# Kernel tuning notes

Measured on AMD Instinct MI355X. Metric: run time of the kernel, lower is better.

The kernel has to match this reference:

```python
import jax, jax.numpy as jnp
import numpy as np

NF = 128  # latent_dim / number of filters


def setup_inputs() -> dict:
    key = jax.random.key(0)
    k1, k2, k3, k4 = jax.random.split(key, 4)
    B, H, W, C = 4, 64, 64, 128
    x = jax.random.normal(k1, (B, H, W, C), dtype=jnp.float32)
    y = jax.random.normal(k2, (B, H, W, C), dtype=jnp.float32)
    # 1x1 conv kernels (C_in, C_out) + biases, glorot-ish scale
    scale = 1.0 / np.sqrt(C)
    W1 = jax.random.normal(k3, (C, NF), dtype=jnp.float32) * scale
    W2 = jax.random.normal(k4, (C, NF), dtype=jnp.float32) * scale
    b1 = jnp.zeros((NF,), dtype=jnp.float32)
    b2 = jnp.zeros((NF,), dtype=jnp.float32)
    return {"x": x, "y": y, "W1": W1, "b1": b1, "W2": W2, "b2": b2}


def reference(x, y, W1, b1, W2, b2):
    B, H, Wd, C = x.shape
    hw = H * Wd
    # 1x1 convs == per-pixel matmul
    xq = jnp.einsum('bhwc,cf->bhwf', x, W1) + b1   # conv1(x)
    yk = jnp.einsum('bhwc,cf->bhwf', y, W2) + b2   # conv2(y)
    xq_r = xq.reshape(B, hw, NF)
    yk_r = yk.reshape(B, hw, NF)
    # A_ij = sigmoid(y_i . x_j), full (hw x hw) sigmoid attention
    A = jax.nn.sigmoid(jnp.einsum('bic,bjc->bij', yk_r, xq_r))
    out = jnp.einsum('bij,bjc->bic', A, yk_r).reshape(B, H, Wd, NF)
    # residual add of the *projected* x (matches original: x was overwritten by conv1)
    out = out + xq
    return out
```

## Files before the change

### kernel.cpp

```cpp
#include <hip/hip_runtime.h>
#include <hip/hip_bf16.h>
#include <stdint.h>

typedef float f32x16 __attribute__((ext_vector_type(16)));
typedef float f32x4  __attribute__((ext_vector_type(4)));
typedef short s16x8  __attribute__((ext_vector_type(8)));
typedef unsigned int u32x4 __attribute__((ext_vector_type(4)));

#define HWSZ   4096
#define NBATCH 4
#define LOG2E  1.44269504088896340736f

__device__ __forceinline__ unsigned short f2bf(float f) {
    unsigned u = __builtin_bit_cast(unsigned, f);
    u += 0x7FFFu + ((u >> 16) & 1u);
    return (unsigned short)(u >> 16);
}
__device__ __forceinline__ unsigned cvt_pk_bf16(float lo, float hi) {
    __hip_bfloat162 h = __float22bfloat162_rn(make_float2(lo, hi));
    return *reinterpret_cast<unsigned*>(&h);
}

__global__ __launch_bounds__(256, 1) void proj_kernel(
    const float* __restrict__ x, const float* __restrict__ y,
    const float* __restrict__ W1, const float* __restrict__ b1,
    const float* __restrict__ W2, const float* __restrict__ b2,
    float* __restrict__ xq_f32,
    unsigned short* __restrict__ xq_bf,
    unsigned short* __restrict__ yk_bf,
    unsigned short* __restrict__ ykT_bf)
{
    __shared__ unsigned short Xlds[64][136];
    __shared__ unsigned short Ylds[64][136];
    __shared__ unsigned short Tlds[128][72];

    const int t    = threadIdx.x;
    const int lane = t & 63;
    const int w    = t >> 6;
    const int l31  = lane & 31;
    const int g    = lane >> 5;
    const int r0   = blockIdx.x * 64;
    const int b    = r0 >> 12;
    const int j0   = r0 & (HWSZ - 1);

    #pragma unroll
    for (int i = 0; i < 8; ++i) {
        int li = t + 256 * i;
        int row = li >> 5, c = (li & 31) * 4;
        float4 vx = *(const float4*)(x + (size_t)(r0 + row) * 128 + c);
        float4 vy = *(const float4*)(y + (size_t)(r0 + row) * 128 + c);
        *(uint2*)&Xlds[row][c] = make_uint2(cvt_pk_bf16(vx.x, vx.y), cvt_pk_bf16(vx.z, vx.w));
        *(uint2*)&Ylds[row][c] = make_uint2(cvt_pk_bf16(vy.x, vy.y), cvt_pk_bf16(vy.z, vy.w));
    }
    __syncthreads();

    const int m  = w >> 1;
    const int fh = w & 1;
    const float* Wm = m ? W2 : W1;
    const float* bm = m ? b2 : b1;
    const unsigned short* A0 = m ? &Ylds[0][0] : &Xlds[0][0];

    f32x16 acc[2][2];
    #pragma unroll
    for (int i = 0; i < 16; ++i) {
        acc[0][0][i] = 0.f; acc[0][1][i] = 0.f;
        acc[1][0][i] = 0.f; acc[1][1][i] = 0.f;
    }

    #pragma unroll
    for (int ks = 0; ks < 8; ++ks) {
        s16x8 bfr[2];
        #pragma unroll
        for (int ft = 0; ft < 2; ++ft) {
            const float* wp = Wm + (size_t)(ks * 16 + g * 8) * 128 + fh * 64 + ft * 32 + l31;
            #pragma unroll
            for (int i = 0; i < 8; ++i)
                bfr[ft][i] = (short)f2bf(wp[(size_t)i * 128]);
        }
        #pragma unroll
        for (int rt = 0; rt < 2; ++rt) {
            s16x8 af = *(const s16x8*)(A0 + (size_t)(rt * 32 + l31) * 136 + ks * 16 + g * 8);
            acc[rt][0] = __builtin_amdgcn_mfma_f32_32x32x16_bf16(af, bfr[0], acc[rt][0], 0, 0, 0);
            acc[rt][1] = __builtin_amdgcn_mfma_f32_32x32x16_bf16(af, bfr[1], acc[rt][1], 0, 0, 0);
        }
    }

    const float bias_v[2] = { bm[fh * 64 + l31], bm[fh * 64 + 32 + l31] };

    if (m == 0) {
        #pragma unroll
        for (int rt = 0; rt < 2; ++rt)
        #pragma unroll
        for (int ft = 0; ft < 2; ++ft) {
            int f = fh * 64 + ft * 32 + l31;
            #pragma unroll
            for (int r = 0; r < 16; ++r) {
                int row = rt * 32 + (r & 3) + 8 * (r >> 2) + 4 * g;
                float v = acc[rt][ft][r] + bias_v[ft];
                size_t o = (size_t)(r0 + row) * 128 + f;
                xq_f32[o] = v;
                xq_bf[o]  = f2bf(v * LOG2E);
            }
        }
    } else {
        #pragma unroll
        for (int rt = 0; rt < 2; ++rt)
        #pragma unroll
        for (int ft = 0; ft < 2; ++ft) {
            int f = fh * 64 + ft * 32 + l31;
            #pragma unroll
            for (int rg = 0; rg < 4; ++rg) {
                float p0 = acc[rt][ft][4 * rg + 0] + bias_v[ft];
                float p1 = acc[rt][ft][4 * rg + 1] + bias_v[ft];
                float p2 = acc[rt][ft][4 * rg + 2] + bias_v[ft];
                float p3 = acc[rt][ft][4 * rg + 3] + bias_v[ft];
                int jb = rt * 32 + 8 * rg + 4 * g;
                *(uint2*)&Tlds[f][jb] = make_uint2(cvt_pk_bf16(p0, p1), cvt_pk_bf16(p2, p3));
                size_t o = (size_t)(r0 + jb) * 128 + f;
                yk_bf[o]       = f2bf(p0);
                yk_bf[o + 128] = f2bf(p1);
                yk_bf[o + 256] = f2bf(p2);
                yk_bf[o + 384] = f2bf(p3);
            }
        }
    }
    __syncthreads();

    {
        int f  = t >> 1;
        int jh = (t & 1) * 32;
        unsigned short* dst = ykT_bf + ((size_t)(b * 128 + f)) * HWSZ + j0 + jh;
        #pragma unroll
        for (int c = 0; c < 4; ++c)
            *(s16x8*)(dst + c * 8) = *(const s16x8*)&Tlds[f][jh + c * 8];
    }
}

#define KT_STR   136
#define VT_STR   72
#define KT_BYTES (64 * KT_STR * 2)
#define VT_BYTES (128 * VT_STR * 2)
#define BUF_BYTES (KT_BYTES + VT_BYTES)

__global__ __launch_bounds__(256, 2) void attn128_kernel(
    const unsigned short* __restrict__ Kbf,
    const unsigned short* __restrict__ Qbf,
    const unsigned short* __restrict__ Vtbf,
    float* __restrict__ outp)
{
    __shared__ __align__(16) char smem[2 * BUF_BYTES];

    const int t    = threadIdx.x;
    const int lane = t & 63;
    const int qt   = t >> 6;
    const int l31  = lane & 31;
    const int g    = lane >> 5;

    const int split  = blockIdx.x >> 7;
    const int r      = blockIdx.x & 127;
    const int b      = r >> 5;
    const int qb     = (r & 31) * 128;
    const int jBegin = split * (HWSZ / 4);
    const int nt     = (HWSZ / 4) / 64;

    s16x8 qfrag[8];
    {
        const unsigned short* qp =
            Qbf + (((size_t)(b * HWSZ + qb + 32 * qt + l31)) << 7) + g * 8;
        #pragma unroll
        for (int fs = 0; fs < 8; ++fs)
            qfrag[fs] = *(const s16x8*)(qp + fs * 16);
    }

    f32x16 acc[4];
    #pragma unroll
    for (int ft = 0; ft < 4; ++ft)
        #pragma unroll
        for (int i = 0; i < 16; ++i) acc[ft][i] = 0.f;

    const unsigned short* Kbase = Kbf  + (((size_t)b * HWSZ) << 7);
    const unsigned short* Vbase = Vtbf + (((size_t)b) << 7) * HWSZ;

    const unsigned short* kSrc = Kbase + (size_t)(jBegin + (t >> 4)) * 128 + (t & 15) * 8;
    const unsigned short* vSrc = Vbase + (size_t)(t >> 3) * HWSZ + jBegin + (t & 7) * 8;
    const int kDst = (t >> 4) * KT_STR + (t & 15) * 8;
    const int vDst = (t >> 3) * VT_STR + (t & 7) * 8;

    {
        unsigned short* Kl = (unsigned short*)smem;
        unsigned short* Vl = (unsigned short*)(smem + KT_BYTES);
        #pragma unroll
        for (int i = 0; i < 4; ++i)
            *(s16x8*)(Kl + kDst + i * 16 * KT_STR) = *(const s16x8*)(kSrc + (size_t)i * 2048);
        #pragma unroll
        for (int i = 0; i < 4; ++i)
            *(s16x8*)(Vl + vDst + i * 32 * VT_STR) = *(const s16x8*)(vSrc + (size_t)i * 32 * HWSZ);
    }
    __syncthreads();

    int c = 0;
    for (int it = 0; it < nt; ++it) {
        const bool pre = (it + 1 < nt);
        s16x8 kr[4], vr[4];
        if (pre) {
            kSrc += 64 * 128;
            vSrc += 64;
            #pragma unroll
            for (int i = 0; i < 4; ++i)
                kr[i] = *(const s16x8*)(kSrc + (size_t)i * 2048);
            #pragma unroll
            for (int i = 0; i < 4; ++i)
                vr[i] = *(const s16x8*)(vSrc + (size_t)i * 32 * HWSZ);
        }

        const unsigned short* Kl = (const unsigned short*)(smem + c * BUF_BYTES);
        const unsigned short* Vl = (const unsigned short*)(smem + c * BUF_BYTES + KT_BYTES);

        #pragma unroll
        for (int jt = 0; jt < 2; ++jt) {
            f32x16 sa, sb;
            #pragma unroll
            for (int i = 0; i < 16; ++i) { sa[i] = 0.f; sb[i] = 0.f; }
            const unsigned short* Krow = Kl + (size_t)(32 * jt + l31) * KT_STR + g * 8;
            __builtin_amdgcn_s_setprio(1);
            #pragma unroll
            for (int fs = 0; fs < 4; ++fs) {
                sa = __builtin_amdgcn_mfma_f32_32x32x16_bf16(
                         *(const s16x8*)(Krow + fs * 16), qfrag[fs], sa, 0, 0, 0);
                sb = __builtin_amdgcn_mfma_f32_32x32x16_bf16(
                         *(const s16x8*)(Krow + (fs + 4) * 16), qfrag[fs + 4], sb, 0, 0, 0);
            }
            __builtin_amdgcn_s_setprio(0);

            unsigned W0[4], W1[4];
            #pragma unroll
            for (int rg = 0; rg < 4; ++rg) {
                float s0 = sa[4 * rg + 0] + sb[4 * rg + 0];
                float s1 = sa[4 * rg + 1] + sb[4 * rg + 1];
                float s2v = sa[4 * rg + 2] + sb[4 * rg + 2];
                float s3 = sa[4 * rg + 3] + sb[4 * rg + 3];
                float p0 = __builtin_amdgcn_rcpf(1.f + __builtin_amdgcn_exp2f(-s0));
                float p1 = __builtin_amdgcn_rcpf(1.f + __builtin_amdgcn_exp2f(-s1));
                float p2 = __builtin_amdgcn_rcpf(1.f + __builtin_amdgcn_exp2f(-s2v));
                float p3 = __builtin_amdgcn_rcpf(1.f + __builtin_amdgcn_exp2f(-s3));
                W0[rg] = cvt_pk_bf16(p0, p1);
                W1[rg] = cvt_pk_bf16(p2, p3);
            }

            #pragma unroll
            for (int s2 = 0; s2 < 2; ++s2) {
                unsigned a0 = W0[2 * s2], b0 = W0[2 * s2 + 1];
                unsigned a1 = W1[2 * s2], b1 = W1[2 * s2 + 1];
                asm("v_permlane32_swap_b32 %0, %1" : "+v"(a0), "+v"(b0));
                asm("v_permlane32_swap_b32 %0, %1" : "+v"(a1), "+v"(b1));
                u32x4 pw;
                pw[0] = a0; pw[1] = a1; pw[2] = b0; pw[3] = b1;
                s16x8 pf = __builtin_bit_cast(s16x8, pw);
                const int ks = 2 * jt + s2;
                __builtin_amdgcn_s_setprio(1);
                #pragma unroll
                for (int ft = 0; ft < 4; ++ft) {
                    s16x8 vf = *(const s16x8*)(Vl + (size_t)(32 * ft + l31) * VT_STR + ks * 16 + g * 8);
                    acc[ft] = __builtin_amdgcn_mfma_f32_32x32x16_bf16(pf, vf, acc[ft], 0, 0, 0);
                }
                __builtin_amdgcn_s_setprio(0);
            }
        }

        if (pre) {
            unsigned short* Kd = (unsigned short*)(smem + (c ^ 1) * BUF_BYTES);
            unsigned short* Vd = (unsigned short*)(smem + (c ^ 1) * BUF_BYTES + KT_BYTES);
            #pragma unroll
            for (int i = 0; i < 4; ++i)
                *(s16x8*)(Kd + kDst + i * 16 * KT_STR) = kr[i];
            #pragma unroll
            for (int i = 0; i < 4; ++i)
                *(s16x8*)(Vd + vDst + i * 32 * VT_STR) = vr[i];
        }
        __syncthreads();
        c ^= 1;
    }

    float* op = outp + (size_t)split * ((size_t)NBATCH * HWSZ * 128);
    #pragma unroll
    for (int ft = 0; ft < 4; ++ft)
    #pragma unroll
    for (int r2 = 0; r2 < 16; ++r2) {
        int row = (r2 & 3) + 8 * (r2 >> 2) + 4 * g;
        int q = qb + 32 * qt + row;
        size_t o = (((size_t)(b * HWSZ + q)) << 7) + 32 * ft + l31;
        op[o] = acc[ft][r2];
    }
}

template<bool SPLIT>
__global__ __launch_bounds__(256, 2) void attn_kernel(
    const unsigned short* __restrict__ Kbf,
    const unsigned short* __restrict__ Qbf,
    const unsigned short* __restrict__ Vtbf,
    const float* __restrict__ resid,
    float* __restrict__ outp)
{
    __shared__ __align__(16) char smem[2 * BUF_BYTES];

    const int t    = threadIdx.x;
    const int lane = t & 63;
    const int w    = t >> 6;
    const int qt   = w & 1;
    const int jt   = w >> 1;
    const int l31  = lane & 31;
    const int g    = lane >> 5;

    int bid = blockIdx.x;
    int half = 0;
    if (SPLIT) { half = bid >> 8; bid &= 255; }
    const int b      = bid >> 6;
    const int qb     = (bid & 63) * 64;
    const int jBegin = half * (HWSZ / 2);
    const int nt     = (SPLIT ? HWSZ / 2 : HWSZ) / 64;

    s16x8 qfrag[8];
    {
        const unsigned short* qp =
            Qbf + (((size_t)(b * HWSZ + qb + 32 * qt + l31)) << 7) + g * 8;
        #pragma unroll
        for (int fs = 0; fs < 8; ++fs)
            qfrag[fs] = *(const s16x8*)(qp + fs * 16);
    }

    f32x16 acc[4];
    #pragma unroll
    for (int ft = 0; ft < 4; ++ft)
        #pragma unroll
        for (int i = 0; i < 16; ++i) acc[ft][i] = 0.f;

    const unsigned short* Kbase = Kbf  + (((size_t)b * HWSZ) << 7);
    const unsigned short* Vbase = Vtbf + (((size_t)b) << 7) * HWSZ;

    const unsigned short* kSrc = Kbase + (size_t)(jBegin + (t >> 4)) * 128 + (t & 15) * 8;
    const unsigned short* vSrc = Vbase + (size_t)(t >> 3) * HWSZ + jBegin + (t & 7) * 8;
    const int kDst = (t >> 4) * KT_STR + (t & 15) * 8;
    const int vDst = (t >> 3) * VT_STR + (t & 7) * 8;

    {
        unsigned short* Kl = (unsigned short*)smem;
        unsigned short* Vl = (unsigned short*)(smem + KT_BYTES);
        #pragma unroll
        for (int i = 0; i < 4; ++i)
            *(s16x8*)(Kl + kDst + i * 16 * KT_STR) = *(const s16x8*)(kSrc + (size_t)i * 2048);
        #pragma unroll
        for (int i = 0; i < 4; ++i)
            *(s16x8*)(Vl + vDst + i * 32 * VT_STR) = *(const s16x8*)(vSrc + (size_t)i * 32 * HWSZ);
    }
    __syncthreads();

    int c = 0;
    for (int it = 0; it < nt; ++it) {
        const bool pre = (it + 1 < nt);
        s16x8 kr[4], vr[4];
        if (pre) {
            kSrc += 64 * 128;
            vSrc += 64;
            #pragma unroll
            for (int i = 0; i < 4; ++i)
                kr[i] = *(const s16x8*)(kSrc + (size_t)i * 2048);
            #pragma unroll
            for (int i = 0; i < 4; ++i)
                vr[i] = *(const s16x8*)(vSrc + (size_t)i * 32 * HWSZ);
        }

        const unsigned short* Kl = (const unsigned short*)(smem + c * BUF_BYTES);
        const unsigned short* Vl = (const unsigned short*)(smem + c * BUF_BYTES + KT_BYTES);

        f32x16 sa, sb;
        #pragma unroll
        for (int i = 0; i < 16; ++i) { sa[i] = 0.f; sb[i] = 0.f; }
        const unsigned short* Krow = Kl + (size_t)(32 * jt + l31) * KT_STR + g * 8;
        __builtin_amdgcn_s_setprio(1);
        #pragma unroll
        for (int fs = 0; fs < 4; ++fs) {
            sa = __builtin_amdgcn_mfma_f32_32x32x16_bf16(
                     *(const s16x8*)(Krow + fs * 16), qfrag[fs], sa, 0, 0, 0);
            sb = __builtin_amdgcn_mfma_f32_32x32x16_bf16(
                     *(const s16x8*)(Krow + (fs + 4) * 16), qfrag[fs + 4], sb, 0, 0, 0);
        }
        __builtin_amdgcn_s_setprio(0);

        unsigned W0[4], W1[4];
        #pragma unroll
        for (int rg = 0; rg < 4; ++rg) {
            float s0 = sa[4 * rg + 0] + sb[4 * rg + 0];
            float s1 = sa[4 * rg + 1] + sb[4 * rg + 1];
            float s2v = sa[4 * rg + 2] + sb[4 * rg + 2];
            float s3 = sa[4 * rg + 3] + sb[4 * rg + 3];
            float p0 = __builtin_amdgcn_rcpf(1.f + __builtin_amdgcn_exp2f(-s0));
            float p1 = __builtin_amdgcn_rcpf(1.f + __builtin_amdgcn_exp2f(-s1));
            float p2 = __builtin_amdgcn_rcpf(1.f + __builtin_amdgcn_exp2f(-s2v));
            float p3 = __builtin_amdgcn_rcpf(1.f + __builtin_amdgcn_exp2f(-s3));
            W0[rg] = cvt_pk_bf16(p0, p1);
            W1[rg] = cvt_pk_bf16(p2, p3);
        }

        #pragma unroll
        for (int s2 = 0; s2 < 2; ++s2) {
            unsigned a0 = W0[2 * s2], b0 = W0[2 * s2 + 1];
            unsigned a1 = W1[2 * s2], b1 = W1[2 * s2 + 1];
            asm("v_permlane32_swap_b32 %0, %1" : "+v"(a0), "+v"(b0));
            asm("v_permlane32_swap_b32 %0, %1" : "+v"(a1), "+v"(b1));
            u32x4 pw;
            pw[0] = a0; pw[1] = a1; pw[2] = b0; pw[3] = b1;
            s16x8 pf = __builtin_bit_cast(s16x8, pw);
            const int ks = 2 * jt + s2;
            __builtin_amdgcn_s_setprio(1);
            #pragma unroll
            for (int ft = 0; ft < 4; ++ft) {
                s16x8 vf = *(const s16x8*)(Vl + (size_t)(32 * ft + l31) * VT_STR + ks * 16 + g * 8);
                acc[ft] = __builtin_amdgcn_mfma_f32_32x32x16_bf16(pf, vf, acc[ft], 0, 0, 0);
            }
            __builtin_amdgcn_s_setprio(0);
        }

        if (pre) {
            unsigned short* Kd = (unsigned short*)(smem + (c ^ 1) * BUF_BYTES);
            unsigned short* Vd = (unsigned short*)(smem + (c ^ 1) * BUF_BYTES + KT_BYTES);
            #pragma unroll
            for (int i = 0; i < 4; ++i)
                *(s16x8*)(Kd + kDst + i * 16 * KT_STR) = kr[i];
            #pragma unroll
            for (int i = 0; i < 4; ++i)
                *(s16x8*)(Vd + vDst + i * 32 * VT_STR) = vr[i];
        }
        __syncthreads();
        c ^= 1;
    }

    float* red = (float*)smem;
    if (jt == 1) {
        #pragma unroll
        for (int ft = 0; ft < 4; ++ft)
        #pragma unroll
        for (int r = 0; r < 16; ++r) {
            int row = (r & 3) + 8 * (r >> 2) + 4 * g;
            red[qt * 4096 + row * 128 + 32 * ft + l31] = acc[ft][r];
        }
    }
    __syncthreads();
    if (jt == 0) {
        float* op = outp + (SPLIT ? (size_t)half * ((size_t)NBATCH * HWSZ * 128) : 0);
        #pragma unroll
        for (int ft = 0; ft < 4; ++ft)
        #pragma unroll
        for (int r = 0; r < 16; ++r) {
            int row = (r & 3) + 8 * (r >> 2) + 4 * g;
            float v = acc[ft][r] + red[qt * 4096 + row * 128 + 32 * ft + l31];
            int q = qb + 32 * qt + row;
            size_t o = (((size_t)(b * HWSZ + q)) << 7) + 32 * ft + l31;
            if (SPLIT) op[o] = v;
            else       op[o] = v + resid[o];
        }
    }
}

__global__ __launch_bounds__(256, 1) void reduce2_kernel(
    const float* __restrict__ p0, const float* __restrict__ p1, float* outp)
{
    int i = blockIdx.x * 256 + threadIdx.x;
    f32x4 a = ((const f32x4*)p0)[i];
    f32x4 b = ((const f32x4*)p1)[i];
    f32x4 c = ((f32x4*)outp)[i];
    ((f32x4*)outp)[i] = a + b + c;
}

template<int S>
__global__ __launch_bounds__(256, 1) void reduceN_kernel(
    const float* __restrict__ parts, float* __restrict__ outp)
{
    const size_t N4 = (size_t)NBATCH * HWSZ * 128 / 4;
    size_t i = (size_t)blockIdx.x * 256 + threadIdx.x;
    f32x4 s = ((f32x4*)outp)[i];
    #pragma unroll
    for (int k = 0; k < S; ++k)
        s += ((const f32x4*)parts)[i + (size_t)k * N4];
    ((f32x4*)outp)[i] = s;
}

extern "C" void kernel_launch(void* const* d_in, const int* in_sizes, int n_in,
                              void* d_out, int out_size, void* d_ws, size_t ws_size,
                              hipStream_t stream) {
    const float* x  = (const float*)d_in[0];
    const float* y  = (const float*)d_in[1];
    const float* W1 = (const float*)d_in[2];
    const float* b1 = (const float*)d_in[3];
    const float* W2 = (const float*)d_in[4];
    const float* b2 = (const float*)d_in[5];
    float* out = (float*)d_out;

    const size_t NELEM = (size_t)NBATCH * HWSZ * 128;
    unsigned short* xq_bf  = (unsigned short*)d_ws;
    unsigned short* yk_bf  = xq_bf + NELEM;
    unsigned short* ykT_bf = yk_bf + NELEM;
    float* part = (float*)(ykT_bf + NELEM);

    proj_kernel<<<(int)(NBATCH * HWSZ / 64), 256, 0, stream>>>(
        x, y, W1, b1, W2, b2, out, xq_bf, yk_bf, ykT_bf);

    if (ws_size >= NELEM * (6 + 16)) {
        attn128_kernel<<<512, 256, 0, stream>>>(xq_bf, yk_bf, ykT_bf, part);
        reduceN_kernel<4><<<(int)(NELEM / 1024), 256, 0, stream>>>(part, out);
    } else if (ws_size >= NELEM * (6 + 8)) {
        attn_kernel<true><<<512, 256, 0, stream>>>(xq_bf, yk_bf, ykT_bf, out, part);
        reduce2_kernel<<<(int)(NELEM / 1024), 256, 0, stream>>>(part, part + NELEM, out);
    } else {
        attn_kernel<false><<<256, 256, 0, stream>>>(xq_bf, yk_bf, ykT_bf, out, out);
    }
}
```

Measured before the change: 69.53 us.

## Split attention key range six ways with single-buffered K to fit three blocks per CU

Adds an attention kernel that splits the key dimension into six uneven chunks (11 or 10 tiles of 64) and launches 768 blocks instead of 512. K shared memory is single-buffered while V stays double-buffered, shrinking LDS so three blocks can reside per CU, and an extra barrier guards the K overwrite. The aim is better CU fill and latency hiding on the 256-CU device. In exchange it writes six fp32 partial outputs and the reduction reads six instead of four, costing extra memory traffic and an added sync per tile. It is only taken when the workspace is large enough.

Measured after the change: 96.87 us. +39.3%, slower.

```diff
diff --git a/kernel.cpp b/kernel.cpp
--- a/kernel.cpp
+++ b/kernel.cpp
@@ -142,13 +142,14 @@
 #define VT_BYTES (128 * VT_STR * 2)
 #define BUF_BYTES (KT_BYTES + VT_BYTES)
 
-__global__ __launch_bounds__(256, 2) void attn128_kernel(
+__global__ __launch_bounds__(256, 3) void attn128s6_kernel(
     const unsigned short* __restrict__ Kbf,
     const unsigned short* __restrict__ Qbf,
     const unsigned short* __restrict__ Vtbf,
     float* __restrict__ outp)
 {
-    __shared__ __align__(16) char smem[2 * BUF_BYTES];
+    __shared__ __align__(16) unsigned short Klds[64 * KT_STR];
+    __shared__ __align__(16) unsigned short Vlds[2][128 * VT_STR];
 
     const int t    = threadIdx.x;
     const int lane = t & 63;
@@ -156,12 +157,13 @@
     const int l31  = lane & 31;
     const int g    = lane >> 5;
 
-    const int split  = blockIdx.x >> 7;
-    const int r      = blockIdx.x & 127;
-    const int b      = r >> 5;
-    const int qb     = (r & 31) * 128;
-    const int jBegin = split * (HWSZ / 4);
-    const int nt     = (HWSZ / 4) / 64;
+    const int split = blockIdx.x >> 7;
+    const int r     = blockIdx.x & 127;
+    const int b     = r >> 5;
+    const int qb    = (r & 31) * 128;
+    const int st    = 11 * split - (split > 4 ? split - 4 : 0);
+    const int nt    = (split >= 4) ? 10 : 11;
+    const int jBegin = st * 64;
 
     s16x8 qfrag[8];
     {
@@ -187,14 +189,12 @@
     const int vDst = (t >> 3) * VT_STR + (t & 7) * 8;
 
     {
-        unsigned short* Kl = (unsigned short*)smem;
-        unsigned short* Vl = (unsigned short*)(smem + KT_BYTES);
         #pragma unroll
         for (int i = 0; i < 4; ++i)
-            *(s16x8*)(Kl + kDst + i * 16 * KT_STR) = *(const s16x8*)(kSrc + (size_t)i * 2048);
+            *(s16x8*)(Klds + kDst + i * 16 * KT_STR) = *(const s16x8*)(kSrc + (size_t)i * 2048);
         #pragma unroll
         for (int i = 0; i < 4; ++i)
-            *(s16x8*)(Vl + vDst + i * 32 * VT_STR) = *(const s16x8*)(vSrc + (size_t)i * 32 * HWSZ);
+            *(s16x8*)(&Vlds[0][0] + vDst + i * 32 * VT_STR) = *(const s16x8*)(vSrc + (size_t)i * 32 * HWSZ);
     }
     __syncthreads();
 
@@ -213,15 +213,14 @@
                 vr[i] = *(const s16x8*)(vSrc + (size_t)i * 32 * HWSZ);
         }
 
-        const unsigned short* Kl = (const unsigned short*)(smem + c * BUF_BYTES);
-        const unsigned short* Vl = (const unsigned short*)(smem + c * BUF_BYTES + KT_BYTES);
+        const unsigned short* Vl = &Vlds[c][0];
 
         #pragma unroll
         for (int jt = 0; jt < 2; ++jt) {
             f32x16 sa, sb;
             #pragma unroll
             for (int i = 0; i < 16; ++i) { sa[i] = 0.f; sb[i] = 0.f; }
-            const unsigned short* Krow = Kl + (size_t)(32 * jt + l31) * KT_STR + g * 8;
+            const unsigned short* Krow = Klds + (size_t)(32 * jt + l31) * KT_STR + g * 8;
             __builtin_amdgcn_s_setprio(1);
             #pragma unroll
             for (int fs = 0; fs < 4; ++fs) {
@@ -267,6 +266,156 @@
             }
         }
 
+        __syncthreads();
+        if (pre) {
+            #pragma unroll
+            for (int i = 0; i < 4; ++i)
+                *(s16x8*)(Klds + kDst + i * 16 * KT_STR) = kr[i];
+            #pragma unroll
+            for (int i = 0; i < 4; ++i)
+                *(s16x8*)(&Vlds[c ^ 1][0] + vDst + i * 32 * VT_STR) = vr[i];
+            __syncthreads();
+        }
+        c ^= 1;
+    }
+
+    float* op = outp + (size_t)split * ((size_t)NBATCH * HWSZ * 128);
+    #pragma unroll
+    for (int ft = 0; ft < 4; ++ft)
+    #pragma unroll
+    for (int r2 = 0; r2 < 16; ++r2) {
+        int row = (r2 & 3) + 8 * (r2 >> 2) + 4 * g;
+        int q = qb + 32 * qt + row;
+        size_t o = (((size_t)(b * HWSZ + q)) << 7) + 32 * ft + l31;
+        op[o] = acc[ft][r2];
+    }
+}
+
+__global__ __launch_bounds__(256, 2) void attn128_kernel(
+    const unsigned short* __restrict__ Kbf,
+    const unsigned short* __restrict__ Qbf,
+    const unsigned short* __restrict__ Vtbf,
+    float* __restrict__ outp)
+{
+    __shared__ __align__(16) char smem[2 * BUF_BYTES];
+
+    const int t    = threadIdx.x;
+    const int lane = t & 63;
+    const int qt   = t >> 6;
+    const int l31  = lane & 31;
+    const int g    = lane >> 5;
+
+    const int split  = blockIdx.x >> 7;
+    const int r      = blockIdx.x & 127;
+    const int b      = r >> 5;
+    const int qb     = (r & 31) * 128;
+    const int jBegin = split * (HWSZ / 4);
+    const int nt     = (HWSZ / 4) / 64;
+
+    s16x8 qfrag[8];
+    {
+        const unsigned short* qp =
+            Qbf + (((size_t)(b * HWSZ + qb + 32 * qt + l31)) << 7) + g * 8;
+        #pragma unroll
+        for (int fs = 0; fs < 8; ++fs)
+            qfrag[fs] = *(const s16x8*)(qp + fs * 16);
+    }
+
+    f32x16 acc[4];
+    #pragma unroll
+    for (int ft = 0; ft < 4; ++ft)
+        #pragma unroll
+        for (int i = 0; i < 16; ++i) acc[ft][i] = 0.f;
+
+    const unsigned short* Kbase = Kbf  + (((size_t)b * HWSZ) << 7);
+    const unsigned short* Vbase = Vtbf + (((size_t)b) << 7) * HWSZ;
+
+    const unsigned short* kSrc = Kbase + (size_t)(jBegin + (t >> 4)) * 128 + (t & 15) * 8;
+    const unsigned short* vSrc = Vbase + (size_t)(t >> 3) * HWSZ + jBegin + (t & 7) * 8;
+    const int kDst = (t >> 4) * KT_STR + (t & 15) * 8;
+    const int vDst = (t >> 3) * VT_STR + (t & 7) * 8;
+
+    {
+        unsigned short* Kl = (unsigned short*)smem;
+        unsigned short* Vl = (unsigned short*)(smem + KT_BYTES);
+        #pragma unroll
+        for (int i = 0; i < 4; ++i)
+            *(s16x8*)(Kl + kDst + i * 16 * KT_STR) = *(const s16x8*)(kSrc + (size_t)i * 2048);
+        #pragma unroll
+        for (int i = 0; i < 4; ++i)
+            *(s16x8*)(Vl + vDst + i * 32 * VT_STR) = *(const s16x8*)(vSrc + (size_t)i * 32 * HWSZ);
+    }
+    __syncthreads();
+
+    int c = 0;
+    for (int it = 0; it < nt; ++it) {
+        const bool pre = (it + 1 < nt);
+        s16x8 kr[4], vr[4];
+        if (pre) {
+            kSrc += 64 * 128;
+            vSrc += 64;
+            #pragma unroll
+            for (int i = 0; i < 4; ++i)
+                kr[i] = *(const s16x8*)(kSrc + (size_t)i * 2048);
+            #pragma unroll
+            for (int i = 0; i < 4; ++i)
+                vr[i] = *(const s16x8*)(vSrc + (size_t)i * 32 * HWSZ);
+        }
+
+        const unsigned short* Kl = (const unsigned short*)(smem + c * BUF_BYTES);
+        const unsigned short* Vl = (const unsigned short*)(smem + c * BUF_BYTES + KT_BYTES);
+
+        #pragma unroll
+        for (int jt = 0; jt < 2; ++jt) {
+            f32x16 sa, sb;
+            #pragma unroll
+            for (int i = 0; i < 16; ++i) { sa[i] = 0.f; sb[i] = 0.f; }
+            const unsigned short* Krow = Kl + (size_t)(32 * jt + l31) * KT_STR + g * 8;
+            __builtin_amdgcn_s_setprio(1);
+            #pragma unroll
+            for (int fs = 0; fs < 4; ++fs) {
+                sa = __builtin_amdgcn_mfma_f32_32x32x16_bf16(
+                         *(const s16x8*)(Krow + fs * 16), qfrag[fs], sa, 0, 0, 0);
+                sb = __builtin_amdgcn_mfma_f32_32x32x16_bf16(
+                         *(const s16x8*)(Krow + (fs + 4) * 16), qfrag[fs + 4], sb, 0, 0, 0);
+            }
+            __builtin_amdgcn_s_setprio(0);
+
+            unsigned W0[4], W1[4];
+            #pragma unroll
+            for (int rg = 0; rg < 4; ++rg) {
+                float s0 = sa[4 * rg + 0] + sb[4 * rg + 0];
+                float s1 = sa[4 * rg + 1] + sb[4 * rg + 1];
+                float s2v = sa[4 * rg + 2] + sb[4 * rg + 2];
+                float s3 = sa[4 * rg + 3] + sb[4 * rg + 3];
+                float p0 = __builtin_amdgcn_rcpf(1.f + __builtin_amdgcn_exp2f(-s0));
+                float p1 = __builtin_amdgcn_rcpf(1.f + __builtin_amdgcn_exp2f(-s1));
+                float p2 = __builtin_amdgcn_rcpf(1.f + __builtin_amdgcn_exp2f(-s2v));
+                float p3 = __builtin_amdgcn_rcpf(1.f + __builtin_amdgcn_exp2f(-s3));
+                W0[rg] = cvt_pk_bf16(p0, p1);
+                W1[rg] = cvt_pk_bf16(p2, p3);
+            }
+
+            #pragma unroll
+            for (int s2 = 0; s2 < 2; ++s2) {
+                unsigned a0 = W0[2 * s2], b0 = W0[2 * s2 + 1];
+                unsigned a1 = W1[2 * s2], b1 = W1[2 * s2 + 1];
+                asm("v_permlane32_swap_b32 %0, %1" : "+v"(a0), "+v"(b0));
+                asm("v_permlane32_swap_b32 %0, %1" : "+v"(a1), "+v"(b1));
+                u32x4 pw;
+                pw[0] = a0; pw[1] = a1; pw[2] = b0; pw[3] = b1;
+                s16x8 pf = __builtin_bit_cast(s16x8, pw);
+                const int ks = 2 * jt + s2;
+                __builtin_amdgcn_s_setprio(1);
+                #pragma unroll
+                for (int ft = 0; ft < 4; ++ft) {
+                    s16x8 vf = *(const s16x8*)(Vl + (size_t)(32 * ft + l31) * VT_STR + ks * 16 + g * 8);
+                    acc[ft] = __builtin_amdgcn_mfma_f32_32x32x16_bf16(pf, vf, acc[ft], 0, 0, 0);
+                }
+                __builtin_amdgcn_s_setprio(0);
+            }
+        }
+
         if (pre) {
             unsigned short* Kd = (unsigned short*)(smem + (c ^ 1) * BUF_BYTES);
             unsigned short* Vd = (unsigned short*)(smem + (c ^ 1) * BUF_BYTES + KT_BYTES);
@@ -504,7 +653,10 @@
     proj_kernel<<<(int)(NBATCH * HWSZ / 64), 256, 0, stream>>>(
         x, y, W1, b1, W2, b2, out, xq_bf, yk_bf, ykT_bf);
 
-    if (ws_size >= NELEM * (6 + 16)) {
+    if (ws_size >= NELEM * (6 + 24)) {
+        attn128s6_kernel<<<768, 256, 0, stream>>>(xq_bf, yk_bf, ykT_bf, part);
+        reduceN_kernel<6><<<(int)(NELEM / 1024), 256, 0, stream>>>(part, out);
+    } else if (ws_size >= NELEM * (6 + 16)) {
         attn128_kernel<<<512, 256, 0, stream>>>(xq_bf, yk_bf, ykT_bf, part);
         reduceN_kernel<4><<<(int)(NELEM / 1024), 256, 0, stream>>>(part, out);
     } else if (ws_size >= NELEM * (6 + 8)) {
```
